# Performance work log

Measured on AMD Instinct MI355X. Metric: run time of the kernel, lower is better.

The kernel has to match this reference:

```python
import jax, jax.numpy as jnp
import numpy as np

B, S, I, H, C, V = 128, 128, 300, 1024, 2, 50000


def setup_inputs() -> dict:
    key = jax.random.key(0)
    ks = jax.random.split(key, 9)
    return {
        "x": jax.random.randint(ks[0], (B, S), 0, V),
        "lengths": jax.random.randint(ks[1], (B,), 1, S + 1),
        "embed_W": jax.random.normal(ks[2], (V, I), jnp.float32) * 0.1,
        "W_ih": jax.random.normal(ks[3], (4 * H, I), jnp.float32) * 0.02,
        "W_hh": jax.random.normal(ks[4], (4 * H, H), jnp.float32) * 0.02,
        "b_ih": jax.random.normal(ks[5], (4 * H,), jnp.float32) * 0.02,
        "b_hh": jax.random.normal(ks[6], (4 * H,), jnp.float32) * 0.02,
        "lin_W": jax.random.normal(ks[7], (C, H), jnp.float32) * 0.02,
        "lin_b": jax.random.normal(ks[8], (C,), jnp.float32) * 0.02,
    }


def reference(x, lengths, embed_W, W_ih, W_hh, b_ih, b_hh, lin_W, lin_b):
    # x: [B, S] int -> time-major embedded input [S, B, I]
    xe = embed_W[x.T]  # [S, B, I]

    def step(carry, xt):
        h, c = carry  # [B, H] each
        gates = xt @ W_ih.T + b_ih + h @ W_hh.T + b_hh  # [B, 4H]
        i_g, f_g, g_g, o_g = jnp.split(gates, 4, axis=-1)  # torch LSTMCell order: i,f,g,o
        c = jax.nn.sigmoid(f_g) * c + jax.nn.sigmoid(i_g) * jnp.tanh(g_g)
        h = jax.nn.sigmoid(o_g) * jnp.tanh(c)
        return (h, c), h

    h0 = jnp.zeros((x.shape[0], W_hh.shape[1]), xe.dtype)
    (_, _), hs = jax.lax.scan(step, (h0, h0), xe)  # hs: [S, B, H]

    out = hs @ lin_W.T + lin_b  # [S, B, C]
    out = out.transpose(1, 0, 2)  # [B, S, C]
    # positions j >= lengths[i] are overwritten with [1, 0]
    valid = (jnp.arange(out.shape[1])[None, :] < lengths[:, None])[..., None]  # [B, S, 1]
    fill = jnp.array([1.0, 0.0], out.dtype)
    out = jnp.where(valid, out, fill)
    return out.reshape(-1, out.shape[-1])  # [B*S, C]
```

## Files before the change

### kernel.cpp

```cpp
#include <hip/hip_runtime.h>
#include <hip/hip_bf16.h>
#include <hip/hip_fp16.h>

#define B_ 128
#define S_ 128
#define I_ 300
#define H_ 1024
#define C_ 2

typedef __attribute__((ext_vector_type(8))) short short8;
typedef __attribute__((ext_vector_type(4))) float f32x4;

__device__ inline short f2b(float f) {
    union { __hip_bfloat16 h; unsigned short s; } cv;
    cv.h = __float2bfloat16(f);
    return (short)cv.s;
}

__global__ __launch_bounds__(256) void prep_bias(
    const float* __restrict__ b_ih, const float* __restrict__ b_hh,
    float* __restrict__ bias)
{
    int i = blockIdx.x * 256 + threadIdx.x;
    if (i < 4 * H_) bias[i] = b_ih[i] + b_hh[i];
}

__global__ __launch_bounds__(256) void prep_wfrag(
    const float* __restrict__ W_hh,
    unsigned short* __restrict__ Wfrag)
{
    int idx = blockIdx.x * 256 + threadIdx.x;
    const int lane = idx & 63;
    const int f    = (idx >> 6) & 31;
    const int wid  = (idx >> 11) & 3;
    const int ug   = idx >> 13;
    const int row  = wid * H_ + ug * 16 + (lane & 15);
    const int k0   = f * 32 + (lane >> 4) * 8;
    const float* src = W_hh + (size_t)row * H_ + k0;
    unsigned short* dst = Wfrag + (size_t)idx * 8;
#pragma unroll
    for (int j = 0; j < 8; ++j)
        dst[j] = (unsigned short)f2b(src[j]);
}

__global__ __launch_bounds__(256) void gemm_ih(
    const int* __restrict__ x,
    const float* __restrict__ embed_W,
    const float* __restrict__ W_ih,
    const float* __restrict__ bias,
    __half* __restrict__ gates)
{
    const int tid = threadIdx.x;
    const int wid = tid >> 6, lane = tid & 63;
    const int fr = lane & 15, fq = lane >> 4;
    const int bx = blockIdx.x;
    const int t  = blockIdx.y;

    __shared__ alignas(16) unsigned short As_[128][40];
    __shared__ alignas(16) unsigned short Bs_[128][40];

    const int sr = tid >> 1;
    const int sc = (tid & 1) * 16;
    const int token = x[sr * S_ + t];
    const float* arow = embed_W + (size_t)token * I_;
    const float* brow = W_ih + (size_t)(bx * 128 + sr) * I_;

    f32x4 acc[2][8] = {};

    for (int kc = 0; kc < 10; ++kc) {
        __syncthreads();
        const int k0 = kc * 32 + sc;
#pragma unroll
        for (int half = 0; half < 2; ++half) {
            const int kh = k0 + half * 8;
            short8 av, bv;
            if (kh + 7 < I_) {
                float4 alo = *(const float4*)(arow + kh);
                float4 ahi = *(const float4*)(arow + kh + 4);
                float4 blo = *(const float4*)(brow + kh);
                float4 bhi = *(const float4*)(brow + kh + 4);
                av[0]=f2b(alo.x); av[1]=f2b(alo.y); av[2]=f2b(alo.z); av[3]=f2b(alo.w);
                av[4]=f2b(ahi.x); av[5]=f2b(ahi.y); av[6]=f2b(ahi.z); av[7]=f2b(ahi.w);
                bv[0]=f2b(blo.x); bv[1]=f2b(blo.y); bv[2]=f2b(blo.z); bv[3]=f2b(blo.w);
                bv[4]=f2b(bhi.x); bv[5]=f2b(bhi.y); bv[6]=f2b(bhi.z); bv[7]=f2b(bhi.w);
            } else {
#pragma unroll
                for (int j = 0; j < 8; ++j) {
                    av[j] = (kh + j < I_) ? f2b(arow[kh + j]) : (short)0;
                    bv[j] = (kh + j < I_) ? f2b(brow[kh + j]) : (short)0;
                }
            }
            *(short8*)&As_[sr][sc + half * 8] = av;
            *(short8*)&Bs_[sr][sc + half * 8] = bv;
        }
        __syncthreads();
        short8 bfrag[8];
#pragma unroll
        for (int nt = 0; nt < 8; ++nt)
            bfrag[nt] = *(const short8*)&Bs_[nt * 16 + fr][fq * 8];
#pragma unroll
        for (int mt = 0; mt < 2; ++mt) {
            short8 a = *(const short8*)&As_[wid * 32 + mt * 16 + fr][fq * 8];
#pragma unroll
            for (int nt = 0; nt < 8; ++nt)
                acc[mt][nt] = __builtin_amdgcn_mfma_f32_16x16x32_bf16(
                    a, bfrag[nt], acc[mt][nt], 0, 0, 0);
        }
    }
#pragma unroll
    for (int mt = 0; mt < 2; ++mt) {
        const int m = t * 128 + wid * 32 + mt * 16 + fq * 4;
#pragma unroll
        for (int nt = 0; nt < 8; ++nt) {
            const int n = bx * 128 + nt * 16 + fr;
            const float bs = bias[n];
#pragma unroll
            for (int r = 0; r < 4; ++r)
                gates[(size_t)(m + r) * 4096 + n] =
                    __float2half(acc[mt][nt][r] + bs);
        }
    }
}

__global__ __launch_bounds__(256, 1) void lstm_step_v2(
    const unsigned short* __restrict__ Wfrag,
    const __half* __restrict__ gates_ih,
    float* __restrict__ c_state,
    __hip_bfloat16* __restrict__ hs,
    int t)
{
    const int tid  = threadIdx.x;
    const int wid  = tid >> 6;
    const int lane = tid & 63;
    const int ug = blockIdx.x;
    const int bg = blockIdx.y;
    const int n0 = ug * 16;
    const int fr = lane & 15, fq = lane >> 4;
    const int m0g = bg * 32;

    __shared__ alignas(16) unsigned short As[32][1048];
    __shared__ float Gs[32][65];

    short8 bfr[32];
    {
        const unsigned short* wf =
            Wfrag + ((size_t)((ug * 4 + wid) * 32) * 64 + lane) * 8;
#pragma unroll
        for (int f = 0; f < 32; ++f)
            bfr[f] = *(const short8*)(wf + (size_t)f * 512);
    }

    {
        const __hip_bfloat16* hprev =
            hs + (size_t)t * (B_ * H_) + (size_t)m0g * H_;
#pragma unroll
        for (int i = 0; i < 16; ++i) {
            const int e = i * 256 + tid;
            const int r = e >> 7, ch = (e & 127) * 8;
            *(short8*)&As[r][ch] = *(const short8*)(hprev + r * H_ + ch);
        }
    }
    __syncthreads();

    f32x4 acc0 = {0.f,0.f,0.f,0.f}, acc1 = {0.f,0.f,0.f,0.f};
    {
        const unsigned short* a0p = &As[fr][fq * 8];
        const unsigned short* a1p = &As[16 + fr][fq * 8];
#pragma unroll
        for (int f = 0; f < 32; ++f) {
            short8 a0 = *(const short8*)(a0p + f * 32);
            short8 a1 = *(const short8*)(a1p + f * 32);
            acc0 = __builtin_amdgcn_mfma_f32_16x16x32_bf16(a0, bfr[f], acc0, 0, 0, 0);
            acc1 = __builtin_amdgcn_mfma_f32_16x16x32_bf16(a1, bfr[f], acc1, 0, 0, 0);
        }
    }

    {
        const int col = wid * 16 + fr;
        const int rb = fq * 4;
#pragma unroll
        for (int r = 0; r < 4; ++r) {
            Gs[rb + r][col]      = acc0[r];
            Gs[16 + rb + r][col] = acc1[r];
        }
    }
    __syncthreads();

    {
        const int cm2 = tid >> 3, up = tid & 7;
        const int u0 = 2 * up;
        const size_t rowbase = ((size_t)t * B_ + m0g + cm2) * 4096 + n0;
        const __half2* gih = (const __half2*)(gates_ih + rowbase);
        float2 gi = __half22float2(gih[up]);
        float2 gf = __half22float2(gih[up + 512]);
        float2 gg = __half22float2(gih[up + 1024]);
        float2 go = __half22float2(gih[up + 1536]);
        float gi0 = Gs[cm2][u0]          + gi.x;
        float gi1 = Gs[cm2][u0 + 1]      + gi.y;
        float gf0 = Gs[cm2][16 + u0]     + gf.x;
        float gf1 = Gs[cm2][16 + u0 + 1] + gf.y;
        float gg0 = Gs[cm2][32 + u0]     + gg.x;
        float gg1 = Gs[cm2][32 + u0 + 1] + gg.y;
        float go0 = Gs[cm2][48 + u0]     + go.x;
        float go1 = Gs[cm2][48 + u0 + 1] + go.y;
        float si0 = 1.f / (1.f + __expf(-gi0));
        float sf0 = 1.f / (1.f + __expf(-gf0));
        float so0 = 1.f / (1.f + __expf(-go0));
        float si1 = 1.f / (1.f + __expf(-gi1));
        float sf1 = 1.f / (1.f + __expf(-gf1));
        float so1 = 1.f / (1.f + __expf(-go1));
        float* cp = c_state + (size_t)(m0g + cm2) * H_ + n0 + u0;
        float2 cc = *(float2*)cp;
        cc.x = sf0 * cc.x + si0 * tanhf(gg0);
        cc.y = sf1 * cc.y + si1 * tanhf(gg1);
        *(float2*)cp = cc;
        float h0 = so0 * tanhf(cc.x);
        float h1 = so1 * tanhf(cc.y);
        unsigned int hv =
            (unsigned int)(unsigned short)f2b(h0) |
            ((unsigned int)(unsigned short)f2b(h1) << 16);
        unsigned int* dst = (unsigned int*)
            (hs + (size_t)(t + 1) * (B_ * H_) +
             (size_t)(m0g + cm2) * H_ + n0) + up;
        *dst = hv;
    }
}

__global__ __launch_bounds__(256) void final_linear(
    const __hip_bfloat16* __restrict__ hs,
    const float* __restrict__ lin_W,
    const float* __restrict__ lin_b,
    const int* __restrict__ lengths,
    float* __restrict__ out)
{
    const int wid  = threadIdx.x >> 6;
    const int lane = threadIdx.x & 63;
    const int p = blockIdx.x * 4 + wid;
    const int b = p >> 7;
    const int t = p & 127;
    const __hip_bfloat16* h =
        hs + (size_t)(t + 1) * (B_ * H_) + (size_t)b * H_;
    float s0 = 0.f, s1 = 0.f;
#pragma unroll
    for (int i = 0; i < 16; ++i) {
        int n = lane + 64 * i;
        float hv = __bfloat162float(h[n]);
        s0 += hv * lin_W[n];
        s1 += hv * lin_W[H_ + n];
    }
#pragma unroll
    for (int off = 32; off > 0; off >>= 1) {
        s0 += __shfl_down(s0, off);
        s1 += __shfl_down(s1, off);
    }
    if (lane == 0) {
        float* o = out + (size_t)p * 2;
        if (t < lengths[b]) {
            o[0] = s0 + lin_b[0];
            o[1] = s1 + lin_b[1];
        } else {
            o[0] = 1.0f;
            o[1] = 0.0f;
        }
    }
}

extern "C" void kernel_launch(void* const* d_in, const int* in_sizes, int n_in,
                              void* d_out, int out_size, void* d_ws,
                              size_t ws_size, hipStream_t stream) {
    const int* x              = (const int*)d_in[0];
    const int* lengths        = (const int*)d_in[1];
    const float* embed_W      = (const float*)d_in[2];
    const float* W_ih         = (const float*)d_in[3];
    const float* W_hh         = (const float*)d_in[4];
    const float* b_ih         = (const float*)d_in[5];
    const float* b_hh         = (const float*)d_in[6];
    const float* lin_W        = (const float*)d_in[7];
    const float* lin_b        = (const float*)d_in[8];
    float* out                = (float*)d_out;

    char* ws = (char*)d_ws;
    __hip_bfloat16* hs    = (__hip_bfloat16*)(ws + 0);
    __half* gates         = (__half*)(ws + 33816576);
    float* bias           = (float*)(ws + 168034304);
    unsigned short* Wfrag = (unsigned short*)(ws + 168050688);
    float* c_state        = (float*)(ws + 176439296);

    prep_bias<<<16, 256, 0, stream>>>(b_ih, b_hh, bias);
    prep_wfrag<<<2048, 256, 0, stream>>>(W_hh, Wfrag);
    (void)hipMemsetAsync(hs, 0, (size_t)B_ * H_ * sizeof(__hip_bfloat16), stream);
    (void)hipMemsetAsync(c_state, 0, (size_t)B_ * H_ * sizeof(float), stream);

    gemm_ih<<<dim3(32, 128), 256, 0, stream>>>(x, embed_W, W_ih, bias, gates);

    for (int t = 0; t < S_; ++t) {
        lstm_step_v2<<<dim3(64, 4), 256, 0, stream>>>(
            Wfrag, gates, c_state, hs, t);
    }

    final_linear<<<dim3((B_ * S_) / 4), 256, 0, stream>>>(
        hs, lin_W, lin_b, lengths, out);
}
```

Measured before the change: 1.067 ms.

## Pre-convert GEMM inputs to padded bf16 and store gates in MFMA fragment layout

Result: faster. 979.3 us (-8.3%).

```diff
diff --git a/kernel.cpp b/kernel.cpp
--- a/kernel.cpp
+++ b/kernel.cpp
@@ -5,6 +5,7 @@
 #define B_ 128
 #define S_ 128
 #define I_ 300
+#define IP_ 320
 #define H_ 1024
 #define C_ 2
 
@@ -25,9 +26,30 @@
     if (i < 4 * H_) bias[i] = b_ih[i] + b_hh[i];
 }
 
+__global__ __launch_bounds__(256) void prep_wih(
+    const float* __restrict__ W_ih, unsigned short* __restrict__ Wp)
+{
+    int idx = blockIdx.x * 256 + threadIdx.x;
+    if (idx >= 4096 * IP_) return;
+    int row = idx / IP_, k = idx - row * IP_;
+    Wp[idx] = (k < I_) ? (unsigned short)f2b(W_ih[row * I_ + k]) : 0;
+}
+
+__global__ __launch_bounds__(256) void prep_xe(
+    const int* __restrict__ x, const float* __restrict__ embed_W,
+    unsigned short* __restrict__ xe)
+{
+    int idx = blockIdx.x * 256 + threadIdx.x;
+    if (idx >= S_ * B_ * IP_) return;
+    int k = idx % IP_;
+    int tb = idx / IP_;
+    int b = tb % B_, t = tb / B_;
+    int row = x[b * S_ + t];
+    xe[idx] = (k < I_) ? (unsigned short)f2b(embed_W[(size_t)row * I_ + k]) : 0;
+}
+
 __global__ __launch_bounds__(256) void prep_wfrag(
-    const float* __restrict__ W_hh,
-    unsigned short* __restrict__ Wfrag)
+    const float* __restrict__ W_hh, unsigned short* __restrict__ Wfrag)
 {
     int idx = blockIdx.x * 256 + threadIdx.x;
     const int lane = idx & 63;
@@ -44,11 +66,10 @@
 }
 
 __global__ __launch_bounds__(256) void gemm_ih(
-    const int* __restrict__ x,
-    const float* __restrict__ embed_W,
-    const float* __restrict__ W_ih,
+    const unsigned short* __restrict__ xe,
+    const unsigned short* __restrict__ Wp,
     const float* __restrict__ bias,
-    __half* __restrict__ gates)
+    unsigned short* __restrict__ gates)
 {
     const int tid = threadIdx.x;
     const int wid = tid >> 6, lane = tid & 63;
@@ -61,38 +82,18 @@
 
     const int sr = tid >> 1;
     const int sc = (tid & 1) * 16;
-    const int token = x[sr * S_ + t];
-    const float* arow = embed_W + (size_t)token * I_;
-    const float* brow = W_ih + (size_t)(bx * 128 + sr) * I_;
+    const unsigned short* arow = xe + ((size_t)t * B_ + sr) * IP_;
+    const unsigned short* brow = Wp + (size_t)(bx * 128 + sr) * IP_;
 
     f32x4 acc[2][8] = {};
 
     for (int kc = 0; kc < 10; ++kc) {
         __syncthreads();
         const int k0 = kc * 32 + sc;
-#pragma unroll
-        for (int half = 0; half < 2; ++half) {
-            const int kh = k0 + half * 8;
-            short8 av, bv;
-            if (kh + 7 < I_) {
-                float4 alo = *(const float4*)(arow + kh);
-                float4 ahi = *(const float4*)(arow + kh + 4);
-                float4 blo = *(const float4*)(brow + kh);
-                float4 bhi = *(const float4*)(brow + kh + 4);
-                av[0]=f2b(alo.x); av[1]=f2b(alo.y); av[2]=f2b(alo.z); av[3]=f2b(alo.w);
-                av[4]=f2b(ahi.x); av[5]=f2b(ahi.y); av[6]=f2b(ahi.z); av[7]=f2b(ahi.w);
-                bv[0]=f2b(blo.x); bv[1]=f2b(blo.y); bv[2]=f2b(blo.z); bv[3]=f2b(blo.w);
-                bv[4]=f2b(bhi.x); bv[5]=f2b(bhi.y); bv[6]=f2b(bhi.z); bv[7]=f2b(bhi.w);
-            } else {
-#pragma unroll
-                for (int j = 0; j < 8; ++j) {
-                    av[j] = (kh + j < I_) ? f2b(arow[kh + j]) : (short)0;
-                    bv[j] = (kh + j < I_) ? f2b(brow[kh + j]) : (short)0;
-                }
-            }
-            *(short8*)&As_[sr][sc + half * 8] = av;
-            *(short8*)&Bs_[sr][sc + half * 8] = bv;
-        }
+        *(short8*)&As_[sr][sc]     = *(const short8*)(arow + k0);
+        *(short8*)&As_[sr][sc + 8] = *(const short8*)(arow + k0 + 8);
+        *(short8*)&Bs_[sr][sc]     = *(const short8*)(brow + k0);
+        *(short8*)&Bs_[sr][sc + 8] = *(const short8*)(brow + k0 + 8);
         __syncthreads();
         short8 bfrag[8];
 #pragma unroll
@@ -107,24 +108,24 @@
                     a, bfrag[nt], acc[mt][nt], 0, 0, 0);
         }
     }
-#pragma unroll
-    for (int mt = 0; mt < 2; ++mt) {
-        const int m = t * 128 + wid * 32 + mt * 16 + fq * 4;
-#pragma unroll
-        for (int nt = 0; nt < 8; ++nt) {
-            const int n = bx * 128 + nt * 16 + fr;
-            const float bs = bias[n];
-#pragma unroll
-            for (int r = 0; r < 4; ++r)
-                gates[(size_t)(m + r) * 4096 + n] =
-                    __float2half(acc[mt][nt][r] + bs);
-        }
-    }
-}
-
-__global__ __launch_bounds__(256, 1) void lstm_step_v2(
+    unsigned short* gbase = gates + (size_t)t * 524288 + (size_t)bx * 16384
+                          + fr * 128 + fq * 32 + wid * 8;
+#pragma unroll
+    for (int nt = 0; nt < 8; ++nt) {
+        const float bs = bias[bx * 128 + nt * 16 + fr];
+        short8 pk;
+#pragma unroll
+        for (int r = 0; r < 4; ++r) {
+            pk[r]     = (short)__half_as_ushort(__float2half(acc[0][nt][r] + bs));
+            pk[4 + r] = (short)__half_as_ushort(__float2half(acc[1][nt][r] + bs));
+        }
+        *(short8*)(gbase + nt * 2048) = pk;
+    }
+}
+
+__global__ __launch_bounds__(256, 1) void lstm_step_v3(
     const unsigned short* __restrict__ Wfrag,
-    const __half* __restrict__ gates_ih,
+    const unsigned short* __restrict__ gates,
     float* __restrict__ c_state,
     __hip_bfloat16* __restrict__ hs,
     int t)
@@ -150,6 +151,14 @@
             bfr[f] = *(const short8*)(wf + (size_t)f * 512);
     }
 
+    union { short8 v; __half h[8]; } gih;
+    {
+        const unsigned short* gp = gates + (size_t)t * 524288
+            + (size_t)(wid * 8 + (ug >> 3)) * 16384
+            + (size_t)(ug & 7) * 2048 + fr * 128 + fq * 32 + bg * 8;
+        gih.v = *(const short8*)gp;
+    }
+
     {
         const __hip_bfloat16* hprev =
             hs + (size_t)t * (B_ * H_) + (size_t)m0g * H_;
@@ -175,6 +184,12 @@
         }
     }
 
+#pragma unroll
+    for (int r = 0; r < 4; ++r) {
+        acc0[r] += __half2float(gih.h[r]);
+        acc1[r] += __half2float(gih.h[4 + r]);
+    }
+
     {
         const int col = wid * 16 + fr;
         const int rb = fq * 4;
@@ -189,20 +204,10 @@
     {
         const int cm2 = tid >> 3, up = tid & 7;
         const int u0 = 2 * up;
-        const size_t rowbase = ((size_t)t * B_ + m0g + cm2) * 4096 + n0;
-        const __half2* gih = (const __half2*)(gates_ih + rowbase);
-        float2 gi = __half22float2(gih[up]);
-        float2 gf = __half22float2(gih[up + 512]);
-        float2 gg = __half22float2(gih[up + 1024]);
-        float2 go = __half22float2(gih[up + 1536]);
-        float gi0 = Gs[cm2][u0]          + gi.x;
-        float gi1 = Gs[cm2][u0 + 1]      + gi.y;
-        float gf0 = Gs[cm2][16 + u0]     + gf.x;
-        float gf1 = Gs[cm2][16 + u0 + 1] + gf.y;
-        float gg0 = Gs[cm2][32 + u0]     + gg.x;
-        float gg1 = Gs[cm2][32 + u0 + 1] + gg.y;
-        float go0 = Gs[cm2][48 + u0]     + go.x;
-        float go1 = Gs[cm2][48 + u0 + 1] + go.y;
+        float gi0 = Gs[cm2][u0],      gi1 = Gs[cm2][u0 + 1];
+        float gf0 = Gs[cm2][16 + u0], gf1 = Gs[cm2][16 + u0 + 1];
+        float gg0 = Gs[cm2][32 + u0], gg1 = Gs[cm2][32 + u0 + 1];
+        float go0 = Gs[cm2][48 + u0], go1 = Gs[cm2][48 + u0 + 1];
         float si0 = 1.f / (1.f + __expf(-gi0));
         float sf0 = 1.f / (1.f + __expf(-gf0));
         float so0 = 1.f / (1.f + __expf(-go0));
@@ -281,20 +286,24 @@
 
     char* ws = (char*)d_ws;
     __hip_bfloat16* hs    = (__hip_bfloat16*)(ws + 0);
-    __half* gates         = (__half*)(ws + 33816576);
+    unsigned short* gates = (unsigned short*)(ws + 33816576);
     float* bias           = (float*)(ws + 168034304);
     unsigned short* Wfrag = (unsigned short*)(ws + 168050688);
     float* c_state        = (float*)(ws + 176439296);
+    unsigned short* xe    = (unsigned short*)(ws + 262144);
+    unsigned short* Wp    = (unsigned short*)(ws + 10747904);
 
     prep_bias<<<16, 256, 0, stream>>>(b_ih, b_hh, bias);
+    prep_wih<<<(4096 * IP_ + 255) / 256, 256, 0, stream>>>(W_ih, Wp);
+    prep_xe<<<(S_ * B_ * IP_ + 255) / 256, 256, 0, stream>>>(x, embed_W, xe);
     prep_wfrag<<<2048, 256, 0, stream>>>(W_hh, Wfrag);
     (void)hipMemsetAsync(hs, 0, (size_t)B_ * H_ * sizeof(__hip_bfloat16), stream);
     (void)hipMemsetAsync(c_state, 0, (size_t)B_ * H_ * sizeof(float), stream);
 
-    gemm_ih<<<dim3(32, 128), 256, 0, stream>>>(x, embed_W, W_ih, bias, gates);
+    gemm_ih<<<dim3(32, 128), 256, 0, stream>>>(xe, Wp, bias, gates);
 
     for (int t = 0; t < S_; ++t) {
-        lstm_step_v2<<<dim3(64, 4), 256, 0, stream>>>(
+        lstm_step_v3<<<dim3(64, 4), 256, 0, stream>>>(
             Wfrag, gates, c_state, hs, t);
     }
 
```
